# Kernel optimization log

Hardware: AMD Instinct MI355X
Metric: run time of the kernel (lower is better)

The kernel has to match this reference:

```python
import jax, jax.numpy as jnp
import numpy as np

IN_C, OUT_C = 32, 32
M1 = M2 = M3 = 12
CFT_M1 = CFT_M2 = M1 // 4  # 3
L_SEG, M_CHEB = 8, 6


def cft2d(x, m1, m2, L, M):
    # Piecewise Chebyshev projection along H (L segments, M polys), rFFT along W.
    # x: [N, C, H, W] -> complex [N, C, m1, m2]
    N, C, H, W = x.shape
    seg = H // L
    t = jnp.linspace(-1.0, 1.0, seg)
    theta = jnp.arccos(jnp.clip(t, -1.0, 1.0))
    P = jnp.cos(jnp.arange(M)[:, None] * theta[None, :])  # [M, seg] Chebyshev T_k
    xs = x.reshape(N, C, L, seg, W)
    coef = jnp.einsum('nclsw,ms->nclmw', xs, P) / seg      # [N,C,L,M,W]
    coef = coef.reshape(N, C, L * M, W)[:, :, :m1, :]      # keep first m1 coeffs
    return jnp.fft.rfft(coef, axis=-1)[:, :, :, :m2]       # [N,C,m1,m2] complex


def setup_inputs() -> dict:
    key = jax.random.key(0)
    ks = jax.random.split(key, 16)
    B, H, W, D = 4, 64, 64, 64
    scale = 1.0 / (IN_C * OUT_C)
    wshape = (IN_C, OUT_C, M1, M2, M3)
    inp = {'x': jax.random.normal(ks[0], (B, IN_C, H, W, D), dtype=jnp.float32)}
    for i in range(4):
        inp[f'w{i+1}_re'] = scale * jax.random.uniform(ks[1 + 2 * i], wshape, dtype=jnp.float32)
        inp[f'w{i+1}_im'] = scale * jax.random.uniform(ks[2 + 2 * i], wshape, dtype=jnp.float32)
    cft_flat = IN_C * CFT_M1 * CFT_M2 * 2  # 576
    hidden = (IN_C + OUT_C) * 2            # 128
    inp['mlp_w1'] = 0.02 * jax.random.normal(ks[9], (cft_flat, hidden), dtype=jnp.float32)
    inp['mlp_b1'] = jnp.zeros((hidden,), dtype=jnp.float32)
    inp['mlp_w2'] = 0.02 * jax.random.normal(ks[10], (hidden, OUT_C), dtype=jnp.float32)
    inp['mlp_b2'] = jnp.zeros((OUT_C,), dtype=jnp.float32)
    inp['corr_scale'] = jnp.float32(0.1)
    return inp


def reference(x, w1_re, w1_im, w2_re, w2_im, w3_re, w3_im, w4_re, w4_im,
              mlp_w1, mlp_b1, mlp_w2, mlp_b2, corr_scale):
    B, C, H, W, D = x.shape
    O = mlp_w2.shape[1]
    x_ft = jnp.fft.rfftn(x, axes=(-3, -2, -1))  # [B,C,H,W,D//2+1] complex64

    def mix(xb, wre, wim):
        return jnp.einsum('bixyz,ioxyz->boxyz', xb, wre + 1j * wim)

    out_ft = jnp.zeros((B, O, H, W, D // 2 + 1), dtype=x_ft.dtype)
    out_ft = out_ft.at[:, :, :M1, :M2, :M3].set(mix(x_ft[:, :, :M1, :M2, :M3], w1_re, w1_im))
    out_ft = out_ft.at[:, :, -M1:, :M2, :M3].set(mix(x_ft[:, :, -M1:, :M2, :M3], w2_re, w2_im))
    out_ft = out_ft.at[:, :, :M1, -M2:, :M3].set(mix(x_ft[:, :, :M1, -M2:, :M3], w3_re, w3_im))
    out_ft = out_ft.at[:, :, -M1:, -M2:, :M3].set(mix(x_ft[:, :, -M1:, -M2:, :M3], w4_re, w4_im))
    x_fno = jnp.fft.irfftn(out_ft, s=(H, W, D), axes=(-3, -2, -1))

    # Chebyshev-Fourier correction branch over depth slices
    xs = jnp.transpose(x, (0, 4, 1, 2, 3)).reshape(B * D, C, H, W)
    cft = cft2d(xs, CFT_M1, CFT_M2, L_SEG, M_CHEB)                 # [B*D,C,3,3] complex
    cft_flat = jnp.stack([cft.real, cft.imag], axis=-1).reshape(B * D, -1)  # view_as_real order
    h = jax.nn.gelu(cft_flat @ mlp_w1 + mlp_b1, approximate=False)
    corr = h @ mlp_w2 + mlp_b2                                     # [B*D, O]
    corr = jnp.transpose(corr.reshape(B, D, O), (0, 2, 1))[:, :, None, None, :]  # [B,O,1,1,D]
    return x_fno + corr_scale * corr
```

## Files before the change

kernel.cpp:

```cpp
#include <hip/hip_runtime.h>
#include <math.h>


#define CMUL_STEP(t, u) do { float _nx = (t).x*(u).x - (t).y*(u).y; \
    (t).y = (t).x*(u).y + (t).y*(u).x; (t).x = _nx; } while (0)

static __device__ __forceinline__ void fill_tw(float2* tw, int tid, int nthr) {
    for (int m = tid; m < 64; m += nthr) {
        float s, c;
        sincosf((float)m * 0.09817477042468103f, &s, &c);
        tw[m] = make_float2(c, s);
    }
}

__global__ __launch_bounds__(256) void k_fwd_zy(const float* __restrict__ x,
                                                float2* __restrict__ X2) {
    __shared__ float xt[64 * 68];
    __shared__ __align__(16) float2 z1[64 * 12];
    __shared__ float2 tw[64];
    const int tid = threadIdx.x;
    const int blk = blockIdx.x;
    fill_tw(tw, tid, 256);
    const float4* xrow4 = (const float4*)(x + (size_t)blk * 4096);
    for (int r = 0; r < 4; ++r) {
        int i4 = r * 256 + tid;
        int w = i4 >> 4, d4 = (i4 & 15) << 2;
        float4 v = xrow4[i4];
        *(float4*)&xt[w * 68 + d4] = v;
    }
    __syncthreads();
    {
        const int w = tid >> 2, kz0 = (tid & 3) * 3;
        const float* xr = &xt[w * 68];
        const float x0v = xr[0], x32v = xr[32];
        const float sg = (kz0 & 1) ? -x32v : x32v;
        float2 a0 = make_float2(x0v + sg, 0.f);
        float2 a1 = make_float2(x0v - sg, 0.f);
        float2 a2 = make_float2(x0v + sg, 0.f);
        const float2 u0 = tw[kz0], u1 = tw[kz0 + 1], u2 = tw[kz0 + 2];
        float2 t0 = u0, t1 = u1, t2 = u2;
        for (int d = 1; d < 32; ++d) {
            float xa = xr[d], xb = xr[64 - d];
            float e = xa + xb, o = xa - xb;
            a0.x += e * t0.x; a0.y -= o * t0.y;
            a1.x += e * t1.x; a1.y -= o * t1.y;
            a2.x += e * t2.x; a2.y -= o * t2.y;
            CMUL_STEP(t0, u0); CMUL_STEP(t1, u1); CMUL_STEP(t2, u2);
        }
        z1[w * 12 + kz0]     = a0;
        z1[w * 12 + kz0 + 1] = a1;
        z1[w * 12 + kz0 + 2] = a2;
    }
    __syncthreads();
    float2* xout = X2 + (size_t)blk * 288;
    if (tid < 156) {
        const int ap = tid / 12, kz = tid - (tid / 12) * 12;
        const float2 zw0 = z1[kz];
        const float2 zw32 = z1[32 * 12 + kz];
        const float sg = (ap & 1) ? -1.f : 1.f;
        float2 A  = make_float2(zw0.x + sg * zw32.x, zw0.y + sg * zw32.y);
        float2 Bc = A;
        const float2 u = tw[ap];
        float2 t = u;
        for (int w = 1; w < 32; ++w) {
            float2 za = z1[w * 12 + kz];
            float2 zb = z1[(64 - w) * 12 + kz];
            float Ex = za.x + zb.x, Ey = za.y + zb.y;
            float Ox = za.x - zb.x, Oy = za.y - zb.y;
            A.x  += t.x * Ex + t.y * Oy;  A.y  += t.x * Ey - t.y * Ox;
            Bc.x += t.x * Ex - t.y * Oy;  Bc.y += t.x * Ey + t.y * Ox;
            CMUL_STEP(t, u);
        }
        if (ap <= 11) xout[ap * 12 + kz] = A;
        if (ap >= 1)  xout[(24 - ap) * 12 + kz] = Bc;
    }
}

__global__ __launch_bounds__(256) void k_fwd_x(const float2* __restrict__ X2,
                                               float2* __restrict__ X3) {
    __shared__ __align__(16) float2 s2[64 * 12];
    __shared__ float2 tw[64];
    const int tid = threadIdx.x;
    const int blk = blockIdx.x;
    const int ay = blk % 24, bc = blk / 24;
    fill_tw(tw, tid, 256);
    const float2* src = X2 + (size_t)bc * (64 * 288) + ay * 12;
    for (int i4 = tid; i4 < 384; i4 += 256) {
        int hh = i4 / 6, c4 = i4 - hh * 6;
        ((float4*)&s2[hh * 12])[c4] = ((const float4*)(src + (size_t)hh * 288))[c4];
    }
    __syncthreads();
    float2* dst = X3 + (size_t)bc * 6912 + ay * 12;
    if (tid < 156) {
        const int ap = tid / 12, kz = tid - (tid / 12) * 12;
        const float2 zw0 = s2[kz];
        const float2 zw32 = s2[32 * 12 + kz];
        const float sg = (ap & 1) ? -1.f : 1.f;
        float2 A  = make_float2(zw0.x + sg * zw32.x, zw0.y + sg * zw32.y);
        float2 Bc = A;
        const float2 u = tw[ap];
        float2 t = u;
        for (int hh = 1; hh < 32; ++hh) {
            float2 za = s2[hh * 12 + kz];
            float2 zb = s2[(64 - hh) * 12 + kz];
            float Ex = za.x + zb.x, Ey = za.y + zb.y;
            float Ox = za.x - zb.x, Oy = za.y - zb.y;
            A.x  += t.x * Ex + t.y * Oy;  A.y  += t.x * Ey - t.y * Ox;
            Bc.x += t.x * Ex - t.y * Oy;  Bc.y += t.x * Ey + t.y * Ox;
            CMUL_STEP(t, u);
        }
        if (ap <= 11) dst[ap * 288 + kz] = A;
        if (ap >= 1)  dst[(24 - ap) * 288 + kz] = Bc;
    }
}

__global__ __launch_bounds__(384) void k_mix(const float2* __restrict__ X3,
                                             float2* __restrict__ F,
        const float* __restrict__ w1re, const float* __restrict__ w1im,
        const float* __restrict__ w2re, const float* __restrict__ w2im,
        const float* __restrict__ w3re, const float* __restrict__ w3im,
        const float* __restrict__ w4re, const float* __restrict__ w4im) {
    __shared__ float2 xs[128 * 12];
    const int tid = threadIdx.x;
    const int blk = blockIdx.x;
    const int ax = blk / 24, ay = blk % 24;
    const int cx = ax >= 12 ? 1 : 0, cy = ay >= 12 ? 1 : 0;
    const int m1 = ax - cx * 12, m2 = ay - cy * 12;
    const int sel = cx + cy * 2;
    const float* wre = sel == 0 ? w1re : sel == 1 ? w2re : sel == 2 ? w3re : w4re;
    const float* wim = sel == 0 ? w1im : sel == 1 ? w2im : sel == 2 ? w3im : w4im;
    const size_t moff = (size_t)ax * 288 + (size_t)ay * 12;
    for (int i = tid; i < 1536; i += 384) {
        int bi = i / 12, kz = i - bi * 12;
        xs[i] = X3[(size_t)bi * 6912 + moff + kz];
    }
    __syncthreads();
    const int o = tid / 12, kz = tid - (tid / 12) * 12;
    const int wbase = o * 1728 + m1 * 144 + m2 * 12 + kz;
    float2 A0 = make_float2(0.f, 0.f), A1 = A0, A2 = A0, A3 = A0;
    for (int i = 0; i < 32; ++i) {
        float wr = wre[i * 55296 + wbase];
        float wi = wim[i * 55296 + wbase];
        float2 x0 = xs[i * 12 + kz];
        float2 x1 = xs[(32 + i) * 12 + kz];
        float2 x2 = xs[(64 + i) * 12 + kz];
        float2 x3 = xs[(96 + i) * 12 + kz];
        A0.x += x0.x * wr - x0.y * wi; A0.y += x0.x * wi + x0.y * wr;
        A1.x += x1.x * wr - x1.y * wi; A1.y += x1.x * wi + x1.y * wr;
        A2.x += x2.x * wr - x2.y * wi; A2.y += x2.x * wi + x2.y * wr;
        A3.x += x3.x * wr - x3.y * wi; A3.y += x3.x * wi + x3.y * wr;
    }
    F[(size_t)(0 * 32 + o) * 6912 + moff + kz] = A0;
    F[(size_t)(1 * 32 + o) * 6912 + moff + kz] = A1;
    F[(size_t)(2 * 32 + o) * 6912 + moff + kz] = A2;
    F[(size_t)(3 * 32 + o) * 6912 + moff + kz] = A3;
}

__global__ __launch_bounds__(256) void k_inv_x(const float2* __restrict__ F,
                                               float2* __restrict__ Y1) {
    __shared__ __align__(16) float2 fs[24 * 12];
    __shared__ float2 tw[64];
    const int tid = threadIdx.x;
    const int blk = blockIdx.x;
    const int ay = blk % 24, bo = blk / 24;
    fill_tw(tw, tid, 256);
    const float2* src = F + (size_t)bo * 6912 + ay * 12;
    for (int i4 = tid; i4 < 144; i4 += 256) {
        int ax = i4 / 6, c4 = i4 - ax * 6;
        ((float4*)&fs[ax * 12])[c4] = ((const float4*)(src + (size_t)ax * 288))[c4];
    }
    __syncthreads();
    float2* dst = Y1 + (size_t)bo * (64 * 288) + ay * 12;
    for (int idx = tid; idx < 396; idx += 256) {
        int hp = idx / 12, kz = idx - (idx / 12) * 12;
        float2 f0  = fs[kz];
        float2 f12 = fs[12 * 12 + kz];
        float2 t12 = tw[(52 * hp) & 63];
        float2 A, Bc;
        A.x  = f0.x + f12.x * t12.x - f12.y * t12.y;
        A.y  = f0.y + f12.x * t12.y + f12.y * t12.x;
        Bc.x = f0.x + f12.x * t12.x + f12.y * t12.y;
        Bc.y = f0.y + f12.y * t12.x - f12.x * t12.y;
        const float2 u = tw[hp];
        float2 t = u;
        for (int a = 1; a <= 11; ++a) {
            float2 fa = fs[a * 12 + kz];
            float2 fb = fs[(24 - a) * 12 + kz];
            float Ex = fa.x + fb.x, Ey = fa.y + fb.y;
            float Ox = fa.x - fb.x, Oy = fa.y - fb.y;
            A.x  += t.x * Ex - t.y * Oy;  A.y  += t.x * Ey + t.y * Ox;
            Bc.x += t.x * Ex + t.y * Oy;  Bc.y += t.x * Ey - t.y * Ox;
            CMUL_STEP(t, u);
        }
        dst[hp * 288 + kz] = A;
        if (hp >= 1 && hp <= 31) dst[(64 - hp) * 288 + kz] = Bc;
    }
}

__global__ __launch_bounds__(256) void k_cft(const float* __restrict__ x,
                                             float* __restrict__ cft) {
    __shared__ float2 tw[64];
    __shared__ float red[3 * 64 * 18];
    const int tid = threadIdx.x;
    const int blk = blockIdx.x;
    const int d = tid & 63, q = tid >> 6;
    fill_tw(tw, tid, 256);
    __syncthreads();
    float aR[3][3] = {{0.f}}, aI[3][3] = {{0.f}};
    const float* xb = x + (size_t)blk * 262144;
    for (int wi = 0; wi < 16; ++wi) {
        const int w = q * 16 + wi;
        float c0 = 0.f, c1 = 0.f, c2 = 0.f;
        #pragma unroll
        for (int s = 0; s < 8; ++s) {
            float xv = xb[(size_t)(s * 64 + w) * 64 + d];
            float t = (2.0f * (float)s - 7.0f) * (1.0f / 7.0f);
            c0 += xv;
            c1 += xv * t;
            c2 += xv * (2.0f * t * t - 1.0f);
        }
        c0 *= 0.125f; c1 *= 0.125f; c2 *= 0.125f;
        #pragma unroll
        for (int f = 0; f < 3; ++f) {
            float2 t = tw[(f * w) & 63];
            aR[0][f] += c0 * t.x; aI[0][f] -= c0 * t.y;
            aR[1][f] += c1 * t.x; aI[1][f] -= c1 * t.y;
            aR[2][f] += c2 * t.x; aI[2][f] -= c2 * t.y;
        }
    }
    if (q > 0) {
        float* dst = &red[((q - 1) * 64 + d) * 18];
        #pragma unroll
        for (int k = 0; k < 3; ++k)
            #pragma unroll
            for (int f = 0; f < 3; ++f) {
                dst[k * 6 + f * 2]     = aR[k][f];
                dst[k * 6 + f * 2 + 1] = aI[k][f];
            }
    }
    __syncthreads();
    if (q == 0) {
        #pragma unroll
        for (int qq = 0; qq < 3; ++qq) {
            const float* sr = &red[(qq * 64 + d) * 18];
            #pragma unroll
            for (int k = 0; k < 3; ++k)
                #pragma unroll
                for (int f = 0; f < 3; ++f) {
                    aR[k][f] += sr[k * 6 + f * 2];
                    aI[k][f] += sr[k * 6 + f * 2 + 1];
                }
        }
        const int b = blk >> 5, c = blk & 31;
        float* dst = cft + (size_t)(b * 64 + d) * 576 + c * 18;
        #pragma unroll
        for (int k = 0; k < 3; ++k)
            #pragma unroll
            for (int f = 0; f < 3; ++f) {
                dst[k * 6 + f * 2]     = aR[k][f];
                dst[k * 6 + f * 2 + 1] = aI[k][f];
            }
    }
}

__global__ __launch_bounds__(128) void k_mlp(const float* __restrict__ cft,
                                             const float* __restrict__ w1,
                                             const float* __restrict__ b1,
                                             const float* __restrict__ w2,
                                             const float* __restrict__ b2,
                                             const float* __restrict__ cs,
                                             float* __restrict__ corr) {
    __shared__ float row[576];
    __shared__ float hbuf[128];
    const int n = blockIdx.x;
    const int tid = threadIdx.x;
    for (int i = tid; i < 576; i += 128) row[i] = cft[(size_t)n * 576 + i];
    __syncthreads();
    float acc = b1[tid];
    #pragma unroll 8
    for (int k = 0; k < 576; ++k) acc += row[k] * w1[k * 128 + tid];
    hbuf[tid] = 0.5f * acc * (1.0f + erff(acc * 0.70710678118654752f));
    __syncthreads();
    if (tid < 32) {
        float a2 = b2[tid];
        #pragma unroll 8
        for (int k = 0; k < 128; ++k) a2 += hbuf[k] * w2[k * 32 + tid];
        const int b = n >> 6, d = n & 63;
        corr[(b * 32 + tid) * 64 + d] = a2 * cs[0];
    }
}

__global__ __launch_bounds__(256) void k_inv_yz(const float2* __restrict__ Y1,
                                                const float* __restrict__ corr,
                                                float* __restrict__ out) {
    __shared__ __align__(16) float2 y1[288];
    __shared__ __align__(16) float2 y2[64 * 12];
    __shared__ float2 tw[64];
    __shared__ float corrl[64];
    const int tid = threadIdx.x;
    const int blk = blockIdx.x;
    const int bo = blk >> 6;
    fill_tw(tw, tid, 256);
    {
        const float4* src4 = (const float4*)(Y1 + (size_t)blk * 288);
        for (int i4 = tid; i4 < 144; i4 += 256) ((float4*)y1)[i4] = src4[i4];
    }
    if (tid < 64) corrl[tid] = corr[bo * 64 + tid];
    __syncthreads();
    {
        const int w = tid >> 2, kz0 = (tid & 3) * 3;
        float2 a0 = make_float2(0.f, 0.f), a1 = a0, a2 = a0;
        {
            float2 f0 = y1[kz0], f1 = y1[kz0 + 1], f2 = y1[kz0 + 2];
            a0.x += f0.x; a0.y += f0.y;
            a1.x += f1.x; a1.y += f1.y;
            a2.x += f2.x; a2.y += f2.y;
        }
        {
            float2 t = tw[(52 * w) & 63];
            float2 f0 = y1[144 + kz0], f1 = y1[144 + kz0 + 1], f2 = y1[144 + kz0 + 2];
            a0.x += f0.x * t.x - f0.y * t.y; a0.y += f0.x * t.y + f0.y * t.x;
            a1.x += f1.x * t.x - f1.y * t.y; a1.y += f1.x * t.y + f1.y * t.x;
            a2.x += f2.x * t.x - f2.y * t.y; a2.y += f2.x * t.y + f2.y * t.x;
        }
        const float2 u = tw[w];
        float2 t = u;
        for (int a = 1; a <= 11; ++a) {
            const float2* fa = &y1[a * 12 + kz0];
            const float2* fb = &y1[(24 - a) * 12 + kz0];
            float2 p0 = fa[0], p1 = fa[1], p2 = fa[2];
            float2 q0 = fb[0], q1 = fb[1], q2 = fb[2];
            float Ex, Ey, Ox, Oy;
            Ex = p0.x + q0.x; Ey = p0.y + q0.y; Ox = p0.x - q0.x; Oy = p0.y - q0.y;
            a0.x += t.x * Ex - t.y * Oy; a0.y += t.x * Ey + t.y * Ox;
            Ex = p1.x + q1.x; Ey = p1.y + q1.y; Ox = p1.x - q1.x; Oy = p1.y - q1.y;
            a1.x += t.x * Ex - t.y * Oy; a1.y += t.x * Ey + t.y * Ox;
            Ex = p2.x + q2.x; Ey = p2.y + q2.y; Ox = p2.x - q2.x; Oy = p2.y - q2.y;
            a2.x += t.x * Ex - t.y * Oy; a2.y += t.x * Ey + t.y * Ox;
            CMUL_STEP(t, u);
        }
        y2[w * 12 + kz0]     = a0;
        y2[w * 12 + kz0 + 1] = a1;
        y2[w * 12 + kz0 + 2] = a2;
    }
    float ctw[12], stw[12];
    const int d = tid & 63;
    #pragma unroll
    for (int kz = 0; kz < 12; ++kz) {
        float2 t = tw[(kz * d) & 63];
        float sc = (kz == 0 ? 1.0f : 2.0f) * (1.0f / 262144.0f);
        ctw[kz] = t.x * sc;
        stw[kz] = t.y * sc;
    }
    __syncthreads();
    const float cv = corrl[d];
    float* orow = out + (size_t)blk * 4096;
    const int wq = tid >> 6;
    for (int r = 0; r < 16; ++r) {
        int w = r * 4 + wq;
        const float4* yv = (const float4*)&y2[w * 12];
        float4 p0 = yv[0], p1 = yv[1], p2 = yv[2];
        float4 p3 = yv[3], p4 = yv[4], p5 = yv[5];
        float s = cv;
        s += p0.x * ctw[0]  - p0.y * stw[0];
        s += p0.z * ctw[1]  - p0.w * stw[1];
        s += p1.x * ctw[2]  - p1.y * stw[2];
        s += p1.z * ctw[3]  - p1.w * stw[3];
        s += p2.x * ctw[4]  - p2.y * stw[4];
        s += p2.z * ctw[5]  - p2.w * stw[5];
        s += p3.x * ctw[6]  - p3.y * stw[6];
        s += p3.z * ctw[7]  - p3.w * stw[7];
        s += p4.x * ctw[8]  - p4.y * stw[8];
        s += p4.z * ctw[9]  - p4.w * stw[9];
        s += p5.x * ctw[10] - p5.y * stw[10];
        s += p5.z * ctw[11] - p5.w * stw[11];
        orow[w * 64 + d] = s;
    }
}

extern "C" void kernel_launch(void* const* d_in, const int* in_sizes, int n_in,
                              void* d_out, int out_size, void* d_ws, size_t ws_size,
                              hipStream_t stream) {
    const float* x    = (const float*)d_in[0];
    const float* w1re = (const float*)d_in[1];
    const float* w1im = (const float*)d_in[2];
    const float* w2re = (const float*)d_in[3];
    const float* w2im = (const float*)d_in[4];
    const float* w3re = (const float*)d_in[5];
    const float* w3im = (const float*)d_in[6];
    const float* w4re = (const float*)d_in[7];
    const float* w4im = (const float*)d_in[8];
    const float* mw1  = (const float*)d_in[9];
    const float* mb1  = (const float*)d_in[10];
    const float* mw2  = (const float*)d_in[11];
    const float* mb2  = (const float*)d_in[12];
    const float* cs   = (const float*)d_in[13];
    float* out = (float*)d_out;

    char* ws = (char*)d_ws;
    float2* X2   = (float2*)(ws);
    float2* X3   = (float2*)(ws + 18874368);
    float2* F    = (float2*)(ws + 25952256);
    float*  cft  = (float*) (ws + 33030144);
    float*  corr = (float*) (ws + 33619968);
    float2* Y1   = X2;

    hipLaunchKernelGGL(k_fwd_zy, dim3(8192), dim3(256), 0, stream, x, X2);
    hipLaunchKernelGGL(k_fwd_x,  dim3(3072), dim3(256), 0, stream, X2, X3);
    hipLaunchKernelGGL(k_mix,    dim3(576),  dim3(384), 0, stream, X3, F,
                       w1re, w1im, w2re, w2im, w3re, w3im, w4re, w4im);
    hipLaunchKernelGGL(k_inv_x,  dim3(3072), dim3(256), 0, stream, F, Y1);
    hipLaunchKernelGGL(k_cft,    dim3(128),  dim3(256), 0, stream, x, cft);
    hipLaunchKernelGGL(k_mlp,    dim3(256),  dim3(128), 0, stream,
                       cft, mw1, mb1, mw2, mb2, cs, corr);
    hipLaunchKernelGGL(k_inv_yz, dim3(8192), dim3(256), 0, stream, Y1, corr, out);
}
```

Baseline: 476.3 us.

## Transpose z-stage shared layout and bake twiddles as compile-time constants

Reworks the first forward DFT stage in k_fwd_zy. Each wavefront now handles a fixed group of three kz modes through a templated function whose twiddle factors are constexpr immediates, which replaces the recurrence multiplies. The input tile is stored transposed with padding 65 so that lanes read consecutive w. The z1 buffer is also transposed and the shared twiddle table is dropped in favour of a per-thread sincosf. The aim is fewer multiply and LDS operations and fewer bank conflicts, at the cost of a scalar, bank-strided transposing store and a larger unrolled code body.

```diff
diff --git a/kernel.cpp b/kernel.cpp
--- a/kernel.cpp
+++ b/kernel.cpp
@@ -4,6 +4,27 @@
 
 #define CMUL_STEP(t, u) do { float _nx = (t).x*(u).x - (t).y*(u).y; \
     (t).y = (t).x*(u).y + (t).y*(u).x; (t).x = _nx; } while (0)
+
+constexpr float TW_C[64] = {
+     1.000000000000000f,  0.995184726672197f,  0.980785280403230f,  0.956940335732209f,
+     0.923879532511287f,  0.881921264348355f,  0.831469612302545f,  0.773010453362737f,
+     0.707106781186548f,  0.634393284163645f,  0.555570233019602f,  0.471396736825998f,
+     0.382683432365090f,  0.290284677254462f,  0.195090322016128f,  0.098017140329561f,
+     0.000000000000000f, -0.098017140329561f, -0.195090322016128f, -0.290284677254462f,
+    -0.382683432365090f, -0.471396736825998f, -0.555570233019602f, -0.634393284163645f,
+    -0.707106781186548f, -0.773010453362737f, -0.831469612302545f, -0.881921264348355f,
+    -0.923879532511287f, -0.956940335732209f, -0.980785280403230f, -0.995184726672197f,
+    -1.000000000000000f, -0.995184726672197f, -0.980785280403230f, -0.956940335732209f,
+    -0.923879532511287f, -0.881921264348355f, -0.831469612302545f, -0.773010453362737f,
+    -0.707106781186548f, -0.634393284163645f, -0.555570233019602f, -0.471396736825998f,
+    -0.382683432365090f, -0.290284677254462f, -0.195090322016128f, -0.098017140329561f,
+     0.000000000000000f,  0.098017140329561f,  0.195090322016128f,  0.290284677254462f,
+     0.382683432365090f,  0.471396736825998f,  0.555570233019602f,  0.634393284163645f,
+     0.707106781186548f,  0.773010453362737f,  0.831469612302545f,  0.881921264348355f,
+     0.923879532511287f,  0.956940335732209f,  0.980785280403230f,  0.995184726672197f
+};
+constexpr float twc(int m) { return TW_C[m & 63]; }
+constexpr float tws(int m) { return TW_C[(m + 48) & 63]; }
 
 static __device__ __forceinline__ void fill_tw(float2* tw, int tid, int nthr) {
     for (int m = tid; m < 64; m += nthr) {
@@ -13,58 +34,72 @@
     }
 }
 
+template<int KZ0>
+static __device__ __forceinline__ void zstage_wave(const float* __restrict__ xt,
+                                                   float2* __restrict__ z1k,
+                                                   int w) {
+    const float x0v  = xt[w];
+    const float x32v = xt[32 * 65 + w];
+    float a0x = x0v + (((KZ0    ) & 1) ? -x32v : x32v), a0y = 0.f;
+    float a1x = x0v + (((KZ0 + 1) & 1) ? -x32v : x32v), a1y = 0.f;
+    float a2x = x0v + (((KZ0 + 2) & 1) ? -x32v : x32v), a2y = 0.f;
+    #pragma unroll
+    for (int d = 1; d < 32; ++d) {
+        const float xa = xt[d * 65 + w];
+        const float xb = xt[(64 - d) * 65 + w];
+        const float e = xa + xb, o = xa - xb;
+        a0x += e * twc((KZ0    ) * d);  a0y -= o * tws((KZ0    ) * d);
+        a1x += e * twc((KZ0 + 1) * d);  a1y -= o * tws((KZ0 + 1) * d);
+        a2x += e * twc((KZ0 + 2) * d);  a2y -= o * tws((KZ0 + 2) * d);
+    }
+    z1k[(KZ0    ) * 66 + w] = make_float2(a0x, a0y);
+    z1k[(KZ0 + 1) * 66 + w] = make_float2(a1x, a1y);
+    z1k[(KZ0 + 2) * 66 + w] = make_float2(a2x, a2y);
+}
+
 __global__ __launch_bounds__(256) void k_fwd_zy(const float* __restrict__ x,
                                                 float2* __restrict__ X2) {
-    __shared__ float xt[64 * 68];
-    __shared__ __align__(16) float2 z1[64 * 12];
-    __shared__ float2 tw[64];
-    const int tid = threadIdx.x;
-    const int blk = blockIdx.x;
-    fill_tw(tw, tid, 256);
+    __shared__ float xt[64 * 65];
+    __shared__ __align__(16) float2 z1k[12 * 66];
+    const int tid = threadIdx.x;
+    const int blk = blockIdx.x;
     const float4* xrow4 = (const float4*)(x + (size_t)blk * 4096);
     for (int r = 0; r < 4; ++r) {
         int i4 = r * 256 + tid;
         int w = i4 >> 4, d4 = (i4 & 15) << 2;
         float4 v = xrow4[i4];
-        *(float4*)&xt[w * 68 + d4] = v;
+        xt[(d4 + 0) * 65 + w] = v.x;
+        xt[(d4 + 1) * 65 + w] = v.y;
+        xt[(d4 + 2) * 65 + w] = v.z;
+        xt[(d4 + 3) * 65 + w] = v.w;
     }
     __syncthreads();
     {
-        const int w = tid >> 2, kz0 = (tid & 3) * 3;
-        const float* xr = &xt[w * 68];
-        const float x0v = xr[0], x32v = xr[32];
-        const float sg = (kz0 & 1) ? -x32v : x32v;
-        float2 a0 = make_float2(x0v + sg, 0.f);
-        float2 a1 = make_float2(x0v - sg, 0.f);
-        float2 a2 = make_float2(x0v + sg, 0.f);
-        const float2 u0 = tw[kz0], u1 = tw[kz0 + 1], u2 = tw[kz0 + 2];
-        float2 t0 = u0, t1 = u1, t2 = u2;
-        for (int d = 1; d < 32; ++d) {
-            float xa = xr[d], xb = xr[64 - d];
-            float e = xa + xb, o = xa - xb;
-            a0.x += e * t0.x; a0.y -= o * t0.y;
-            a1.x += e * t1.x; a1.y -= o * t1.y;
-            a2.x += e * t2.x; a2.y -= o * t2.y;
-            CMUL_STEP(t0, u0); CMUL_STEP(t1, u1); CMUL_STEP(t2, u2);
-        }
-        z1[w * 12 + kz0]     = a0;
-        z1[w * 12 + kz0 + 1] = a1;
-        z1[w * 12 + kz0 + 2] = a2;
+        const int q = tid >> 6, w = tid & 63;
+        switch (q) {
+            case 0: zstage_wave<0>(xt, z1k, w); break;
+            case 1: zstage_wave<3>(xt, z1k, w); break;
+            case 2: zstage_wave<6>(xt, z1k, w); break;
+            default: zstage_wave<9>(xt, z1k, w); break;
+        }
     }
     __syncthreads();
     float2* xout = X2 + (size_t)blk * 288;
     if (tid < 156) {
         const int ap = tid / 12, kz = tid - (tid / 12) * 12;
-        const float2 zw0 = z1[kz];
-        const float2 zw32 = z1[32 * 12 + kz];
+        const float2* zr = &z1k[kz * 66];
+        const float2 zw0 = zr[0];
+        const float2 zw32 = zr[32];
         const float sg = (ap & 1) ? -1.f : 1.f;
         float2 A  = make_float2(zw0.x + sg * zw32.x, zw0.y + sg * zw32.y);
         float2 Bc = A;
-        const float2 u = tw[ap];
+        float s_, c_;
+        sincosf((float)ap * 0.09817477042468103f, &s_, &c_);
+        const float2 u = make_float2(c_, s_);
         float2 t = u;
         for (int w = 1; w < 32; ++w) {
-            float2 za = z1[w * 12 + kz];
-            float2 zb = z1[(64 - w) * 12 + kz];
+            float2 za = zr[w];
+            float2 zb = zr[64 - w];
             float Ex = za.x + zb.x, Ey = za.y + zb.y;
             float Ox = za.x - zb.x, Oy = za.y - zb.y;
             A.x  += t.x * Ex + t.y * Oy;  A.y  += t.x * Ey - t.y * Ox;
```

Measured after the change: 468.7 us. No clear change (-1.6%).
